# Kernel optimization log

Measured on AMD Instinct MI355X. Metric: run time of the kernel, lower is better.

## Reference

```python
import jax, jax.numpy as jnp
import numpy as np
from jax.scipy.special import logsumexp

EPS_SINK = 0.1
N_ITERS = 100
LN_EPS = 1e-5
ANAT_W = (1.0, 1.0, 1.2)  # anatomical_weights[0:3] used by _get_region_weights
GRIDS = ((5, 0.2), (15, 0.3), (25, 0.5))  # (grid_size, scale_weight)


def layernorm(x, g, b):
    m = x.mean(-1, keepdims=True)
    v = ((x - m) ** 2).mean(-1, keepdims=True)
    return (x - m) / jnp.sqrt(v + LN_EPS) * g + b


def spatial_distribution(bb, g):
    # bb: [B, D, 4] in 0..1000 coords -> [B, D, g*g] binary occupancy grid
    B, D, _ = bb.shape
    bc = bb * (g / 1000.0)
    x, y, w, h = bc[..., 0], bc[..., 1], bc[..., 2], bc[..., 3]
    x1 = jnp.maximum(jnp.trunc(x), 0.0)          # max(0, int(x))
    y1 = jnp.maximum(jnp.trunc(y), 0.0)
    x2 = jnp.minimum(jnp.trunc(x + w), g - 1.0)  # min(g-1, int(x+w))
    y2 = jnp.minimum(jnp.trunc(y + h), g - 1.0)
    gi = jnp.arange(g, dtype=bb.dtype)
    row = (gi[None, None, :, None] >= y1[..., None, None]) & (gi[None, None, :, None] <= y2[..., None, None])
    col = (gi[None, None, None, :] >= x1[..., None, None]) & (gi[None, None, None, :] <= x2[..., None, None])
    nz = jnp.any(bc != 0, axis=-1)[..., None, None]
    grid = (row & col & nz).astype(bb.dtype)  # [B, D, g, g]
    return grid.reshape(B, D, g * g)


def emd_pairs(d1, d2, g):
    # d1, d2: [B, P, n] spatial distributions; returns [B, P] pseudo-EMD exactly as source
    yy, xx = jnp.meshgrid(jnp.arange(g), jnp.arange(g), indexing='ij')
    pos = jnp.stack([xx.ravel(), yy.ravel()], axis=1).astype(jnp.float32)
    diff = pos[:, None, :] - pos[None, :, :]
    C = jnp.sqrt((diff * diff).sum(-1))
    C = C / C.max()
    rw = jnp.ones((g, g), jnp.float32)
    rw = rw.at[: g // 3].mul(ANAT_W[0]).at[g // 3 : (2 * g) // 3].mul(ANAT_W[1]).at[(2 * g) // 3 :].mul(ANAT_W[2])
    C = C * rw.ravel()  # broadcast over columns, same as torch C[n,n] * weights[n]
    K = jnp.exp(-C / EPS_SINK)
    logP = jnp.log(d1[..., :, None] + 1e-8)  # [B,P,n,1]
    logQ = jnp.log(d2[..., None, :] + 1e-8)  # [B,P,1,n]

    def step(carry, _):
        u, v = carry
        u = logP - logsumexp(v + K, axis=-1, keepdims=True)
        v = logQ - logsumexp(u + K.T, axis=-2, keepdims=True)
        return (u, v), None

    (u, v), _ = jax.lax.scan(step, (jnp.zeros_like(logP), jnp.zeros_like(logQ)), None, length=N_ITERS)
    Pm = jnp.exp(u + v + K)
    return (Pm * C).sum((-2, -1))


def setup_inputs() -> dict:
    key = jax.random.key(0)
    ks = jax.random.split(key, 6)
    B, D, F, Hd = 1, 14, 768, 256
    features = jax.random.normal(ks[0], (B, D, F), jnp.float32)
    # x,y in [0,800), w,h in [0,200) so boxes stay inside the 0..1000 frame
    bb = jax.random.uniform(ks[1], (B, D, 4), jnp.float32) * jnp.array([800.0, 800.0, 200.0, 200.0])
    return {
        'features': features,
        'bb_coords': bb,
        'w_embed': jax.random.normal(ks[2], (F, Hd), jnp.float32) * 0.02,
        'b_embed': jnp.zeros((Hd,), jnp.float32),
        'g1': jnp.ones((Hd,), jnp.float32),
        'b1': jnp.zeros((Hd,), jnp.float32),
        'gat_W': jax.random.normal(ks[3], (3, Hd, Hd), jnp.float32) * 0.02,
        'gat_b': jnp.zeros((3, Hd), jnp.float32),
        'gat_g': jnp.ones((3, Hd), jnp.float32),
        'gat_bt': jnp.zeros((3, Hd), jnp.float32),
        'w_out': jax.random.normal(ks[4], (Hd, F), jnp.float32) * 0.02,
        'b_out': jnp.zeros((F,), jnp.float32),
        'g2': jnp.ones((F,), jnp.float32),
        'b2': jnp.zeros((F,), jnp.float32),
    }


def reference(features, bb_coords, w_embed, b_embed, g1, b1, gat_W, gat_b, gat_g, gat_bt, w_out, b_out, g2, b2):
    B, D, _ = features.shape
    H = 1  # num_heads (the only shape-consistent value for the source module)
    x = layernorm(features @ w_embed + b_embed, g1, b1)

    # --- EMD-based adjacency over all 91 unordered disease pairs, vectorized ---
    iu, ju = np.triu_indices(D, k=1)
    adj = jnp.zeros((B, D, D), features.dtype)
    for g, sw in GRIDS:
        dist = spatial_distribution(bb_coords, g)            # [B, D, g*g]
        emd = emd_pairs(dist[:, iu], dist[:, ju], g)         # [B, 91]
        adj = adj.at[:, iu, ju].add(sw * emd).at[:, ju, iu].add(sw * emd)
    adj = jax.nn.softmax(adj, axis=-1)

    # --- 3 GAT layers (q=k=v, per source) ---
    attns = []
    for l in range(3):
        h = x @ gat_W[l] + gat_b[l]                          # [B, D, 256]
        hd = h.shape[-1] // H
        q = h.reshape(B, D, H, hd).transpose(0, 2, 1, 3)     # [B, H, D, hd]
        attn = jnp.einsum('bhnd,bhmd->bhnm', q, q) * hd ** -0.5
        attn = jnp.where(adj[:, None] == 0, -jnp.inf, attn)
        attn = jax.nn.softmax(attn, axis=-1)
        o = jnp.einsum('bhnm,bhmd->bhnd', attn, q)
        o = o.transpose(0, 2, 1, 3).reshape(B, D, H * hd)
        x = layernorm(o, gat_g[l], gat_bt[l])
        attns.append(attn.mean(1))
        x = jax.nn.elu(x)

    out = layernorm(x @ w_out + b_out, g2, b2)
    final_attention = jnp.stack(attns).mean(0)
    return out, final_attention
```

## Files before the change

### kernel.cpp

```cpp
#include <hip/hip_runtime.h>
#include <math.h>


#define NWG 16

__device__ __forceinline__ void astore(float* p, float v) {
  __hip_atomic_store(p, v, __ATOMIC_RELAXED, __HIP_MEMORY_SCOPE_AGENT);
}

__device__ __forceinline__ void bar_arrive(int* flags, int slot, int w) {
  asm volatile("s_waitcnt vmcnt(0)" ::: "memory");
  __syncthreads();
  if (threadIdx.x == 0)
    __hip_atomic_store(&flags[slot * NWG + w], 1, __ATOMIC_RELAXED,
                       __HIP_MEMORY_SCOPE_AGENT);
}

__device__ __forceinline__ void bar_wait(int* flags, int slot) {
  if (threadIdx.x < NWG) {
    while (__hip_atomic_load(&flags[slot * NWG + threadIdx.x],
                             __ATOMIC_RELAXED,
                             __HIP_MEMORY_SCOPE_AGENT) == 0)
      __builtin_amdgcn_s_sleep(1);
  }
  __syncthreads();
  asm volatile("" ::: "memory");
}

__global__ __launch_bounds__(1024) void sdg_fused(
    const float* __restrict__ feat, const float* __restrict__ w_embed,
    const float* __restrict__ b_embed, const float* __restrict__ g1,
    const float* __restrict__ b1, const float* __restrict__ gat_W,
    const float* __restrict__ gat_b, const float* __restrict__ gat_g,
    const float* __restrict__ gat_bt, const float* __restrict__ w_out,
    const float* __restrict__ b_out, const float* __restrict__ g2,
    const float* __restrict__ b2, float* __restrict__ out, int* flags,
    float* __restrict__ e_ws, float* __restrict__ h_ws,
    float* __restrict__ gp_ws, float* __restrict__ st1_ws,
    float* __restrict__ st2_ws) {
  const int w = blockIdx.x, tid = threadIdx.x;
  const int w16 = w * 16, w48 = w * 48;
  const int c = tid & 15;
  const int ksl = (tid >> 4) & 15;
  const int rg = tid >> 8;
  const int t2 = tid & 255;

  __shared__ __align__(16) float SA[14592];
  __shared__ __align__(16) float SB[10752];
  __shared__ __align__(16) float Pb[3600];
  __shared__ float Hb[240];
  __shared__ float Gm[224];
  __shared__ float Asm[224];
  __shared__ float aRow[224];
  __shared__ float hm[16];
  __shared__ float Ov[686];
  __shared__ float Mn[14], Rs[14], ps[14], psq[14];

  float* const Fs = SB;
  float* const Xs = SB;

#pragma unroll
  for (int i = 0; i < 3; ++i) {
    const int idx = i * 1024 + tid;
    const int k = idx >> 2, q = (idx & 3) * 4;
    const float4 v = *(const float4*)(&w_embed[k * 256 + w16 + q]);
    SA[k * 19 + q + 0] = v.x;
    SA[k * 19 + q + 1] = v.y;
    SA[k * 19 + q + 2] = v.z;
    SA[k * 19 + q + 3] = v.w;
  }
  for (int i = tid; i < 2688; i += 1024)
    *(float4*)(&Fs[i * 4]) = ((const float4*)feat)[i];
  if (tid < 224) aRow[tid] = 0.f;
  if (tid < 28) Asm[(tid >> 1) * 16 + 14 + (tid & 1)] = 0.f;
  if (tid < 2) hm[14 + tid] = 0.f;
  __syncthreads();

  {
    float acc[4] = {0.f, 0.f, 0.f, 0.f};
    const int r0 = rg * 4, kb = ksl * 48;
#pragma unroll
    for (int ch = 0; ch < 12; ++ch) {
      const int k = kb + ch * 4;
      const float w0 = SA[(k + 0) * 19 + c];
      const float w1 = SA[(k + 1) * 19 + c];
      const float w2 = SA[(k + 2) * 19 + c];
      const float w3 = SA[(k + 3) * 19 + c];
#pragma unroll
      for (int rr = 0; rr < 4; ++rr) {
        const int r = r0 + rr;
        if (r < 14) {
          const float4 xv = *(const float4*)(&Fs[r * 768 + k]);
          acc[rr] = fmaf(
              xv.x, w0, fmaf(xv.y, w1, fmaf(xv.z, w2, fmaf(xv.w, w3, acc[rr]))));
        }
      }
    }
#pragma unroll
    for (int rr = 0; rr < 4; ++rr) {
      const int r = r0 + rr;
      if (r < 14) Pb[ksl * 225 + r * 16 + c] = acc[rr];
    }
  }
  __syncthreads();
  if (tid < 224) {
    const int r = tid >> 4, cc = tid & 15;
    float v = b_embed[w16 + cc];
#pragma unroll
    for (int q = 0; q < 16; ++q) v += Pb[q * 225 + tid];
    astore(&e_ws[r * 256 + w16 + cc], v);
    float sv = v, sq = v * v;
#pragma unroll
    for (int off = 8; off; off >>= 1) {
      sv += __shfl_xor(sv, off, 16);
      sq += __shfl_xor(sq, off, 16);
    }
    if (cc == 0) {
      astore(&st1_ws[w * 28 + r], sv);
      astore(&st1_ws[w * 28 + 14 + r], sq);
    }
  }
  bar_arrive(flags, 0, w);
  {
    const int k = tid >> 2, q = (tid & 3) * 4;
    const float4 v = *(const float4*)(&gat_W[k * 256 + w16 + q]);
    SA[k * 19 + q + 0] = v.x;
    SA[k * 19 + q + 1] = v.y;
    SA[k * 19 + q + 2] = v.z;
    SA[k * 19 + q + 3] = v.w;
  }
  bar_wait(flags, 0);

  if (tid < 224) {
    const int r = tid >> 4, seg = tid & 15;
    float S = st1_ws[seg * 28 + r];
    float Q = st1_ws[seg * 28 + 14 + r];
#pragma unroll
    for (int off = 8; off; off >>= 1) {
      S += __shfl_xor(S, off, 16);
      Q += __shfl_xor(Q, off, 16);
    }
    if (seg == 0) {
      const float m = S * (1.f / 256.f);
      Mn[r] = m;
      Rs[r] = rsqrtf(Q * (1.f / 256.f) - m * m + 1e-5f);
    }
  }
  if (tid < 896) {
    const float4 v = ((const float4*)e_ws)[tid];
    const int idx = tid * 4, r = idx >> 8, cc = idx & 255;
    *(float4*)(&Xs[r * 260 + cc]) = v;
  }
  __syncthreads();
  for (int i = tid; i < 3584; i += 1024) {
    const int r = i >> 8, cc = i & 255;
    Xs[r * 260 + cc] = (Xs[r * 260 + cc] - Mn[r]) * Rs[r] * g1[cc] + b1[cc];
  }
  __syncthreads();

  for (int l = 0; l < 3; ++l) {
    {
      float acc[4] = {0.f, 0.f, 0.f, 0.f};
      const int r0 = rg * 4, kb = ksl * 16;
#pragma unroll
      for (int ch = 0; ch < 4; ++ch) {
        const int k = kb + ch * 4;
        const float w0 = SA[(k + 0) * 19 + c];
        const float w1 = SA[(k + 1) * 19 + c];
        const float w2 = SA[(k + 2) * 19 + c];
        const float w3 = SA[(k + 3) * 19 + c];
#pragma unroll
        for (int rr = 0; rr < 4; ++rr) {
          const int r = r0 + rr;
          if (r < 14) {
            const float4 xv = *(const float4*)(&Xs[r * 260 + k]);
            acc[rr] = fmaf(
                xv.x, w0,
                fmaf(xv.y, w1, fmaf(xv.z, w2, fmaf(xv.w, w3, acc[rr]))));
          }
        }
      }
#pragma unroll
      for (int rr = 0; rr < 4; ++rr) {
        const int r = r0 + rr;
        if (r < 14) Pb[ksl * 225 + r * 16 + c] = acc[rr];
      }
    }
    __syncthreads();
    if (tid < 224) {
      const int r = tid >> 4, cc = tid & 15;
      float v = gat_b[l * 256 + w16 + cc];
#pragma unroll
      for (int q = 0; q < 16; ++q) v += Pb[q * 225 + tid];
      Hb[r * 17 + cc] = v;
      astore(&h_ws[l * 3584 + r * 256 + w16 + cc], v);
      float sv = v;
#pragma unroll
      for (int off = 8; off; off >>= 1) sv += __shfl_xor(sv, off, 16);
      if (cc == 0) astore(&gp_ws[l * 3584 + w * 224 + 196 + r], sv);
    }
    __syncthreads();
    if (tid < 196) {
      const int i = tid / 14, j = tid - i * 14;
      float s = 0.f;
#pragma unroll
      for (int cc = 0; cc < 16; ++cc)
        s = fmaf(Hb[i * 17 + cc], Hb[j * 17 + cc], s);
      astore(&gp_ws[l * 3584 + w * 224 + tid], s);
    }
    bar_arrive(flags, 1 + l, w);
    if (l < 2) {
      const float* Wn = gat_W + (l + 1) * 65536;
      const int k = tid >> 2, q = (tid & 3) * 4;
      const float4 v = *(const float4*)(&Wn[k * 256 + w16 + q]);
      SA[k * 19 + q + 0] = v.x;
      SA[k * 19 + q + 1] = v.y;
      SA[k * 19 + q + 2] = v.z;
      SA[k * 19 + q + 3] = v.w;
    } else {
#pragma unroll
      for (int g = 0; g < 3; ++g) {
        const int k = tid >> 2, q = (tid & 3) * 4;
        const float4 v = *(const float4*)(&w_out[k * 768 + w48 + g * 16 + q]);
        SA[g * 4864 + k * 19 + q + 0] = v.x;
        SA[g * 4864 + k * 19 + q + 1] = v.y;
        SA[g * 4864 + k * 19 + q + 2] = v.z;
        SA[g * 4864 + k * 19 + q + 3] = v.w;
      }
    }
    bar_wait(flags, 1 + l);

    float hv[16];
    hv[14] = 0.f;
    hv[15] = 0.f;
#pragma unroll
    for (int m = 0; m < 14; ++m) hv[m] = h_ws[l * 3584 + m * 256 + t2];
    if (tid < 196) {
      float s = 0.f;
      const float* gpl = gp_ws + l * 3584 + tid;
#pragma unroll
      for (int ww = 0; ww < 16; ++ww) s += gpl[ww * 224];
      const int i = tid / 14, j = tid - i * 14;
      Gm[i * 16 + j] = s;
      Asm[i * 16 + j] = s * 0.0625f;
    } else if (tid < 210) {
      const int m = tid - 196;
      float s = 0.f;
      const float* gpl = gp_ws + l * 3584 + 196 + m;
#pragma unroll
      for (int ww = 0; ww < 16; ++ww) s += gpl[ww * 224];
      hm[m] = s * (1.f / 256.f);
    }
    __syncthreads();
    if (tid < 224) {
      const int r = tid >> 4, j = tid & 15;
      const float lv = (j < 14) ? Asm[r * 16 + j] : -1e30f;
      float mx = lv;
#pragma unroll
      for (int off = 8; off; off >>= 1) mx = fmaxf(mx, __shfl_xor(mx, off, 16));
      float p = (j < 14) ? expf(lv - mx) : 0.f;
      float sm = p;
#pragma unroll
      for (int off = 8; off; off >>= 1) sm += __shfl_xor(sm, off, 16);
      p /= sm;
      if (j < 14) {
        Asm[r * 16 + j] = p;
        aRow[r * 16 + j] += p * (1.f / 3.f);
      }
    }
    __syncthreads();
    float o[4] = {0.f, 0.f, 0.f, 0.f};
#pragma unroll
    for (int mc = 0; mc < 4; ++mc) {
#pragma unroll
      for (int rr = 0; rr < 4; ++rr) {
        const int r = rg * 4 + rr;
        if (r < 14) {
          const float4 a = *(const float4*)(&Asm[r * 16 + mc * 4]);
          o[rr] = fmaf(a.x, hv[mc * 4 + 0],
                       fmaf(a.y, hv[mc * 4 + 1],
                            fmaf(a.z, hv[mc * 4 + 2],
                                 fmaf(a.w, hv[mc * 4 + 3], o[rr]))));
        }
      }
    }
    if (tid < 224) {
      const int r = tid >> 4, j = tid & 15;
      const float aj = Asm[r * 16 + j];
      float tq = 0.f;
      if (j < 14) {
#pragma unroll
        for (int i = 0; i < 14; ++i)
          tq = fmaf(Asm[r * 16 + i], Gm[i * 16 + j], tq);
      }
      float qv = tq * aj;
      float mv = aj * hm[j];
#pragma unroll
      for (int off = 8; off; off >>= 1) {
        qv += __shfl_xor(qv, off, 16);
        mv += __shfl_xor(mv, off, 16);
      }
      if (j == 0) {
        Mn[r] = mv;
        Rs[r] = rsqrtf(qv * (1.f / 256.f) - mv * mv + 1e-5f);
      }
    }
    __syncthreads();
    {
      const float gc = gat_g[l * 256 + t2], bc = gat_bt[l * 256 + t2];
#pragma unroll
      for (int rr = 0; rr < 4; ++rr) {
        const int r = rg * 4 + rr;
        if (r < 14) {
          const float xn = (o[rr] - Mn[r]) * Rs[r] * gc + bc;
          Xs[r * 260 + t2] = xn > 0.f ? xn : expm1f(xn);
        }
      }
      if (l == 2) {
        if (w < 14 && tid < 14)
          out[10752 + w * 14 + tid] = aRow[w * 16 + tid];
        if (tid < 14) {
          ps[tid] = 0.f;
          psq[tid] = 0.f;
        }
      }
    }
    __syncthreads();
  }

  for (int g = 0; g < 3; ++g) {
    {
      float acc[4] = {0.f, 0.f, 0.f, 0.f};
      const int r0 = rg * 4, kb = ksl * 16;
#pragma unroll
      for (int ch = 0; ch < 4; ++ch) {
        const int k = kb + ch * 4;
        const float w0 = SA[g * 4864 + (k + 0) * 19 + c];
        const float w1 = SA[g * 4864 + (k + 1) * 19 + c];
        const float w2 = SA[g * 4864 + (k + 2) * 19 + c];
        const float w3 = SA[g * 4864 + (k + 3) * 19 + c];
#pragma unroll
        for (int rr = 0; rr < 4; ++rr) {
          const int r = r0 + rr;
          if (r < 14) {
            const float4 xv = *(const float4*)(&Xs[r * 260 + k]);
            acc[rr] = fmaf(
                xv.x, w0,
                fmaf(xv.y, w1, fmaf(xv.z, w2, fmaf(xv.w, w3, acc[rr]))));
          }
        }
      }
#pragma unroll
      for (int rr = 0; rr < 4; ++rr) {
        const int r = r0 + rr;
        if (r < 14) Pb[ksl * 225 + r * 16 + c] = acc[rr];
      }
    }
    __syncthreads();
    if (tid < 224) {
      const int r = tid >> 4, cc = tid & 15;
      float v = b_out[w48 + g * 16 + cc];
#pragma unroll
      for (int q = 0; q < 16; ++q) v += Pb[q * 225 + tid];
      Ov[r * 49 + g * 16 + cc] = v;
      float sv = v, sq = v * v;
#pragma unroll
      for (int off = 8; off; off >>= 1) {
        sv += __shfl_xor(sv, off, 16);
        sq += __shfl_xor(sq, off, 16);
      }
      if (cc == 0) {
        ps[r] += sv;
        psq[r] += sq;
      }
    }
    __syncthreads();
  }
  if (tid < 14) {
    astore(&st2_ws[w * 28 + tid], ps[tid]);
    astore(&st2_ws[w * 28 + 14 + tid], psq[tid]);
  }
  bar_arrive(flags, 4, w);
  bar_wait(flags, 4);
  if (tid < 224) {
    const int r = tid >> 4, seg = tid & 15;
    float S = st2_ws[seg * 28 + r];
    float Q = st2_ws[seg * 28 + 14 + r];
#pragma unroll
    for (int off = 8; off; off >>= 1) {
      S += __shfl_xor(S, off, 16);
      Q += __shfl_xor(Q, off, 16);
    }
    if (seg == 0) {
      const float m = S * (1.f / 768.f);
      Mn[r] = m;
      Rs[r] = rsqrtf(Q * (1.f / 768.f) - m * m + 1e-5f);
    }
  }
  __syncthreads();
  if (tid < 224) {
    const int r = tid >> 4, cc = tid & 15;
    const float m = Mn[r], rs = Rs[r];
#pragma unroll
    for (int g = 0; g < 3; ++g) {
      const int col = w48 + g * 16 + cc;
      out[r * 768 + col] =
          (Ov[r * 49 + g * 16 + cc] - m) * rs * g2[col] + b2[col];
    }
  }
}

extern "C" void kernel_launch(void* const* d_in, const int* in_sizes, int n_in,
                              void* d_out, int out_size, void* d_ws,
                              size_t ws_size, hipStream_t stream) {
  const float* feat = (const float*)d_in[0];
  const float* w_embed = (const float*)d_in[2];
  const float* b_embed = (const float*)d_in[3];
  const float* g1 = (const float*)d_in[4];
  const float* b1 = (const float*)d_in[5];
  const float* gat_W = (const float*)d_in[6];
  const float* gat_b = (const float*)d_in[7];
  const float* gat_g = (const float*)d_in[8];
  const float* gat_bt = (const float*)d_in[9];
  const float* w_out = (const float*)d_in[10];
  const float* b_out = (const float*)d_in[11];
  const float* g2 = (const float*)d_in[12];
  const float* b2 = (const float*)d_in[13];
  float* out = (float*)d_out;

  int* flags = (int*)d_ws;
  float* e_ws = (float*)d_ws + 96;
  float* h_ws = e_ws + 3584;
  float* gp_ws = h_ws + 3 * 3584;
  float* st1_ws = gp_ws + 3 * 3584;
  float* st2_ws = st1_ws + 448;

  hipMemsetAsync(flags, 0, 96 * sizeof(int), stream);
  sdg_fused<<<NWG, 1024, 0, stream>>>(feat, w_embed, b_embed, g1, b1, gat_W,
                                      gat_b, gat_g, gat_bt, w_out, b_out, g2,
                                      b2, out, flags, e_ws, h_ws, gp_ws,
                                      st1_ws, st2_ws);
}
```

Before: 40.89 us.

## Split fused kernel across 32 workgroups with 8-column slices

Doubles the number of cooperating workgroups from 16 to 32, so each handles 8 output columns instead of 16. The K-split doubles to 32 slices and the partial-sum, workspace and flag layouts are resized to match. The aim is to spread the per-block weight loads and matmul work over more compute units, so each block has less serial work. In exchange, every grid barrier has to wait on twice as many blocks, each cross-block reduction reads twice as many partials, and fewer threads per block do useful work.

```diff
diff --git a/kernel.cpp b/kernel.cpp
--- a/kernel.cpp
+++ b/kernel.cpp
@@ -2,7 +2,7 @@
 #include <math.h>
 
 
-#define NWG 16
+#define NWG 32
 
 __device__ __forceinline__ void astore(float* p, float v) {
   __hip_atomic_store(p, v, __ATOMIC_RELAXED, __HIP_MEMORY_SCOPE_AGENT);
@@ -39,35 +39,37 @@
     float* __restrict__ gp_ws, float* __restrict__ st1_ws,
     float* __restrict__ st2_ws) {
   const int w = blockIdx.x, tid = threadIdx.x;
-  const int w16 = w * 16, w48 = w * 48;
-  const int c = tid & 15;
-  const int ksl = (tid >> 4) & 15;
+  const int w8 = w * 8, w24 = w * 24;
+  const int c = tid & 7;
+  const int ksl = (tid >> 3) & 31;
   const int rg = tid >> 8;
   const int t2 = tid & 255;
 
-  __shared__ __align__(16) float SA[14592];
+  __shared__ __align__(16) float SA[6912];
   __shared__ __align__(16) float SB[10752];
-  __shared__ __align__(16) float Pb[3600];
-  __shared__ float Hb[240];
+  __shared__ __align__(16) float Pb[3616];
+  __shared__ float Hb[126];
   __shared__ float Gm[224];
   __shared__ float Asm[224];
   __shared__ float aRow[224];
   __shared__ float hm[16];
-  __shared__ float Ov[686];
+  __shared__ float Ov[350];
   __shared__ float Mn[14], Rs[14], ps[14], psq[14];
 
   float* const Fs = SB;
   float* const Xs = SB;
 
 #pragma unroll
-  for (int i = 0; i < 3; ++i) {
+  for (int i = 0; i < 2; ++i) {
     const int idx = i * 1024 + tid;
-    const int k = idx >> 2, q = (idx & 3) * 4;
-    const float4 v = *(const float4*)(&w_embed[k * 256 + w16 + q]);
-    SA[k * 19 + q + 0] = v.x;
-    SA[k * 19 + q + 1] = v.y;
-    SA[k * 19 + q + 2] = v.z;
-    SA[k * 19 + q + 3] = v.w;
+    if (idx < 1536) {
+      const int k = idx >> 1, q = (idx & 1) * 4;
+      const float4 v = *(const float4*)(&w_embed[k * 256 + w8 + q]);
+      SA[k * 9 + q + 0] = v.x;
+      SA[k * 9 + q + 1] = v.y;
+      SA[k * 9 + q + 2] = v.z;
+      SA[k * 9 + q + 3] = v.w;
+    }
   }
   for (int i = tid; i < 2688; i += 1024)
     *(float4*)(&Fs[i * 4]) = ((const float4*)feat)[i];
@@ -78,14 +80,14 @@
 
   {
     float acc[4] = {0.f, 0.f, 0.f, 0.f};
-    const int r0 = rg * 4, kb = ksl * 48;
-#pragma unroll
-    for (int ch = 0; ch < 12; ++ch) {
+    const int r0 = rg * 4, kb = ksl * 24;
+#pragma unroll
+    for (int ch = 0; ch < 6; ++ch) {
       const int k = kb + ch * 4;
-      const float w0 = SA[(k + 0) * 19 + c];
-      const float w1 = SA[(k + 1) * 19 + c];
-      const float w2 = SA[(k + 2) * 19 + c];
-      const float w3 = SA[(k + 3) * 19 + c];
+      const float w0 = SA[(k + 0) * 9 + c];
+      const float w1 = SA[(k + 1) * 9 + c];
+      const float w2 = SA[(k + 2) * 9 + c];
+      const float w3 = SA[(k + 3) * 9 + c];
 #pragma unroll
       for (int rr = 0; rr < 4; ++rr) {
         const int r = r0 + rr;
@@ -99,21 +101,21 @@
 #pragma unroll
     for (int rr = 0; rr < 4; ++rr) {
       const int r = r0 + rr;
-      if (r < 14) Pb[ksl * 225 + r * 16 + c] = acc[rr];
-    }
-  }
-  __syncthreads();
-  if (tid < 224) {
-    const int r = tid >> 4, cc = tid & 15;
-    float v = b_embed[w16 + cc];
-#pragma unroll
-    for (int q = 0; q < 16; ++q) v += Pb[q * 225 + tid];
-    astore(&e_ws[r * 256 + w16 + cc], v);
+      if (r < 14) Pb[ksl * 113 + r * 8 + c] = acc[rr];
+    }
+  }
+  __syncthreads();
+  if (tid < 112) {
+    const int r = tid >> 3, cc = tid & 7;
+    float v = b_embed[w8 + cc];
+#pragma unroll
+    for (int q = 0; q < 32; ++q) v += Pb[q * 113 + tid];
+    astore(&e_ws[r * 256 + w8 + cc], v);
     float sv = v, sq = v * v;
 #pragma unroll
-    for (int off = 8; off; off >>= 1) {
-      sv += __shfl_xor(sv, off, 16);
-      sq += __shfl_xor(sq, off, 16);
+    for (int off = 4; off; off >>= 1) {
+      sv += __shfl_xor(sv, off, 8);
+      sq += __shfl_xor(sq, off, 8);
     }
     if (cc == 0) {
       astore(&st1_ws[w * 28 + r], sv);
@@ -121,24 +123,24 @@
     }
   }
   bar_arrive(flags, 0, w);
-  {
-    const int k = tid >> 2, q = (tid & 3) * 4;
-    const float4 v = *(const float4*)(&gat_W[k * 256 + w16 + q]);
-    SA[k * 19 + q + 0] = v.x;
-    SA[k * 19 + q + 1] = v.y;
-    SA[k * 19 + q + 2] = v.z;
-    SA[k * 19 + q + 3] = v.w;
+  if (tid < 512) {
+    const int k = tid >> 1, q = (tid & 1) * 4;
+    const float4 v = *(const float4*)(&gat_W[k * 256 + w8 + q]);
+    SA[k * 9 + q + 0] = v.x;
+    SA[k * 9 + q + 1] = v.y;
+    SA[k * 9 + q + 2] = v.z;
+    SA[k * 9 + q + 3] = v.w;
   }
   bar_wait(flags, 0);
 
-  if (tid < 224) {
-    const int r = tid >> 4, seg = tid & 15;
+  if (tid < 448) {
+    const int r = tid >> 5, seg = tid & 31;
     float S = st1_ws[seg * 28 + r];
     float Q = st1_ws[seg * 28 + 14 + r];
 #pragma unroll
-    for (int off = 8; off; off >>= 1) {
-      S += __shfl_xor(S, off, 16);
-      Q += __shfl_xor(Q, off, 16);
+    for (int off = 16; off; off >>= 1) {
+      S += __shfl_xor(S, off, 32);
+      Q += __shfl_xor(Q, off, 32);
     }
     if (seg == 0) {
       const float m = S * (1.f / 256.f);
@@ -161,14 +163,14 @@
   for (int l = 0; l < 3; ++l) {
     {
       float acc[4] = {0.f, 0.f, 0.f, 0.f};
-      const int r0 = rg * 4, kb = ksl * 16;
-#pragma unroll
-      for (int ch = 0; ch < 4; ++ch) {
+      const int r0 = rg * 4, kb = ksl * 8;
+#pragma unroll
+      for (int ch = 0; ch < 2; ++ch) {
         const int k = kb + ch * 4;
-        const float w0 = SA[(k + 0) * 19 + c];
-        const float w1 = SA[(k + 1) * 19 + c];
-        const float w2 = SA[(k + 2) * 19 + c];
-        const float w3 = SA[(k + 3) * 19 + c];
+        const float w0 = SA[(k + 0) * 9 + c];
+        const float w1 = SA[(k + 1) * 9 + c];
+        const float w2 = SA[(k + 2) * 9 + c];
+        const float w3 = SA[(k + 3) * 9 + c];
 #pragma unroll
         for (int rr = 0; rr < 4; ++rr) {
           const int r = r0 + rr;
@@ -183,49 +185,53 @@
 #pragma unroll
       for (int rr = 0; rr < 4; ++rr) {
         const int r = r0 + rr;
-        if (r < 14) Pb[ksl * 225 + r * 16 + c] = acc[rr];
-      }
-    }
-    __syncthreads();
-    if (tid < 224) {
-      const int r = tid >> 4, cc = tid & 15;
-      float v = gat_b[l * 256 + w16 + cc];
-#pragma unroll
-      for (int q = 0; q < 16; ++q) v += Pb[q * 225 + tid];
-      Hb[r * 17 + cc] = v;
-      astore(&h_ws[l * 3584 + r * 256 + w16 + cc], v);
+        if (r < 14) Pb[ksl * 113 + r * 8 + c] = acc[rr];
+      }
+    }
+    __syncthreads();
+    if (tid < 112) {
+      const int r = tid >> 3, cc = tid & 7;
+      float v = gat_b[l * 256 + w8 + cc];
+#pragma unroll
+      for (int q = 0; q < 32; ++q) v += Pb[q * 113 + tid];
+      Hb[r * 9 + cc] = v;
+      astore(&h_ws[l * 3584 + r * 256 + w8 + cc], v);
       float sv = v;
 #pragma unroll
-      for (int off = 8; off; off >>= 1) sv += __shfl_xor(sv, off, 16);
-      if (cc == 0) astore(&gp_ws[l * 3584 + w * 224 + 196 + r], sv);
+      for (int off = 4; off; off >>= 1) sv += __shfl_xor(sv, off, 8);
+      if (cc == 0) astore(&gp_ws[l * 7168 + w * 224 + 196 + r], sv);
     }
     __syncthreads();
     if (tid < 196) {
       const int i = tid / 14, j = tid - i * 14;
       float s = 0.f;
 #pragma unroll
-      for (int cc = 0; cc < 16; ++cc)
-        s = fmaf(Hb[i * 17 + cc], Hb[j * 17 + cc], s);
-      astore(&gp_ws[l * 3584 + w * 224 + tid], s);
+      for (int cc = 0; cc < 8; ++cc)
+        s = fmaf(Hb[i * 9 + cc], Hb[j * 9 + cc], s);
+      astore(&gp_ws[l * 7168 + w * 224 + tid], s);
     }
     bar_arrive(flags, 1 + l, w);
     if (l < 2) {
-      const float* Wn = gat_W + (l + 1) * 65536;
-      const int k = tid >> 2, q = (tid & 3) * 4;
-      const float4 v = *(const float4*)(&Wn[k * 256 + w16 + q]);
-      SA[k * 19 + q + 0] = v.x;
-      SA[k * 19 + q + 1] = v.y;
-      SA[k * 19 + q + 2] = v.z;
-      SA[k * 19 + q + 3] = v.w;
+      if (tid < 512) {
+        const float* Wn = gat_W + (l + 1) * 65536;
+        const int k = tid >> 1, q = (tid & 1) * 4;
+        const float4 v = *(const float4*)(&Wn[k * 256 + w8 + q]);
+        SA[k * 9 + q + 0] = v.x;
+        SA[k * 9 + q + 1] = v.y;
+        SA[k * 9 + q + 2] = v.z;
+        SA[k * 9 + q + 3] = v.w;
+      }
     } else {
-#pragma unroll
-      for (int g = 0; g < 3; ++g) {
-        const int k = tid >> 2, q = (tid & 3) * 4;
-        const float4 v = *(const float4*)(&w_out[k * 768 + w48 + g * 16 + q]);
-        SA[g * 4864 + k * 19 + q + 0] = v.x;
-        SA[g * 4864 + k * 19 + q + 1] = v.y;
-        SA[g * 4864 + k * 19 + q + 2] = v.z;
-        SA[g * 4864 + k * 19 + q + 3] = v.w;
+      if (tid < 512) {
+        const int k = tid >> 1, q = (tid & 1) * 4;
+#pragma unroll
+        for (int g = 0; g < 3; ++g) {
+          const float4 v = *(const float4*)(&w_out[k * 768 + w24 + g * 8 + q]);
+          SA[g * 2304 + k * 9 + q + 0] = v.x;
+          SA[g * 2304 + k * 9 + q + 1] = v.y;
+          SA[g * 2304 + k * 9 + q + 2] = v.z;
+          SA[g * 2304 + k * 9 + q + 3] = v.w;
+        }
       }
     }
     bar_wait(flags, 1 + l);
@@ -237,18 +243,18 @@
     for (int m = 0; m < 14; ++m) hv[m] = h_ws[l * 3584 + m * 256 + t2];
     if (tid < 196) {
       float s = 0.f;
-      const float* gpl = gp_ws + l * 3584 + tid;
-#pragma unroll
-      for (int ww = 0; ww < 16; ++ww) s += gpl[ww * 224];
+      const float* gpl = gp_ws + l * 7168 + tid;
+#pragma unroll
+      for (int ww = 0; ww < 32; ++ww) s += gpl[ww * 224];
       const int i = tid / 14, j = tid - i * 14;
       Gm[i * 16 + j] = s;
       Asm[i * 16 + j] = s * 0.0625f;
     } else if (tid < 210) {
       const int m = tid - 196;
       float s = 0.f;
-      const float* gpl = gp_ws + l * 3584 + 196 + m;
-#pragma unroll
-      for (int ww = 0; ww < 16; ++ww) s += gpl[ww * 224];
+      const float* gpl = gp_ws + l * 7168 + 196 + m;
+#pragma unroll
+      for (int ww = 0; ww < 32; ++ww) s += gpl[ww * 224];
       hm[m] = s * (1.f / 256.f);
     }
     __syncthreads();
@@ -331,14 +337,14 @@
   for (int g = 0; g < 3; ++g) {
     {
       float acc[4] = {0.f, 0.f, 0.f, 0.f};
-      const int r0 = rg * 4, kb = ksl * 16;
-#pragma unroll
-      for (int ch = 0; ch < 4; ++ch) {
+      const int r0 = rg * 4, kb = ksl * 8;
+#pragma unroll
+      for (int ch = 0; ch < 2; ++ch) {
         const int k = kb + ch * 4;
-        const float w0 = SA[g * 4864 + (k + 0) * 19 + c];
-        const float w1 = SA[g * 4864 + (k + 1) * 19 + c];
-        const float w2 = SA[g * 4864 + (k + 2) * 19 + c];
-        const float w3 = SA[g * 4864 + (k + 3) * 19 + c];
+        const float w0 = SA[g * 2304 + (k + 0) * 9 + c];
+        const float w1 = SA[g * 2304 + (k + 1) * 9 + c];
+        const float w2 = SA[g * 2304 + (k + 2) * 9 + c];
+        const float w3 = SA[g * 2304 + (k + 3) * 9 + c];
 #pragma unroll
         for (int rr = 0; rr < 4; ++rr) {
           const int r = r0 + rr;
@@ -353,21 +359,21 @@
 #pragma unroll
       for (int rr = 0; rr < 4; ++rr) {
         const int r = r0 + rr;
-        if (r < 14) Pb[ksl * 225 + r * 16 + c] = acc[rr];
-      }
-    }
-    __syncthreads();
-    if (tid < 224) {
-      const int r = tid >> 4, cc = tid & 15;
-      float v = b_out[w48 + g * 16 + cc];
-#pragma unroll
-      for (int q = 0; q < 16; ++q) v += Pb[q * 225 + tid];
-      Ov[r * 49 + g * 16 + cc] = v;
+        if (r < 14) Pb[ksl * 113 + r * 8 + c] = acc[rr];
+      }
+    }
+    __syncthreads();
+    if (tid < 112) {
+      const int r = tid >> 3, cc = tid & 7;
+      float v = b_out[w24 + g * 8 + cc];
+#pragma unroll
+      for (int q = 0; q < 32; ++q) v += Pb[q * 113 + tid];
+      Ov[r * 25 + g * 8 + cc] = v;
       float sv = v, sq = v * v;
 #pragma unroll
-      for (int off = 8; off; off >>= 1) {
-        sv += __shfl_xor(sv, off, 16);
-        sq += __shfl_xor(sq, off, 16);
+      for (int off = 4; off; off >>= 1) {
+        sv += __shfl_xor(sv, off, 8);
+        sq += __shfl_xor(sq, off, 8);
       }
       if (cc == 0) {
         ps[r] += sv;
@@ -382,14 +388,14 @@
   }
   bar_arrive(flags, 4, w);
   bar_wait(flags, 4);
-  if (tid < 224) {
-    const int r = tid >> 4, seg = tid & 15;
+  if (tid < 448) {
+    const int r = tid >> 5, seg = tid & 31;
     float S = st2_ws[seg * 28 + r];
     float Q = st2_ws[seg * 28 + 14 + r];
 #pragma unroll
-    for (int off = 8; off; off >>= 1) {
-      S += __shfl_xor(S, off, 16);
-      Q += __shfl_xor(Q, off, 16);
+    for (int off = 16; off; off >>= 1) {
+      S += __shfl_xor(S, off, 32);
+      Q += __shfl_xor(Q, off, 32);
     }
     if (seg == 0) {
       const float m = S * (1.f / 768.f);
@@ -398,14 +404,14 @@
     }
   }
   __syncthreads();
-  if (tid < 224) {
-    const int r = tid >> 4, cc = tid & 15;
+  if (tid < 112) {
+    const int r = tid >> 3, cc = tid & 7;
     const float m = Mn[r], rs = Rs[r];
 #pragma unroll
     for (int g = 0; g < 3; ++g) {
-      const int col = w48 + g * 16 + cc;
+      const int col = w24 + g * 8 + cc;
       out[r * 768 + col] =
-          (Ov[r * 49 + g * 16 + cc] - m) * rs * g2[col] + b2[col];
+          (Ov[r * 25 + g * 8 + cc] - m) * rs * g2[col] + b2[col];
     }
   }
 }
@@ -429,13 +435,13 @@
   float* out = (float*)d_out;
 
   int* flags = (int*)d_ws;
-  float* e_ws = (float*)d_ws + 96;
+  float* e_ws = (float*)d_ws + 192;
   float* h_ws = e_ws + 3584;
   float* gp_ws = h_ws + 3 * 3584;
-  float* st1_ws = gp_ws + 3 * 3584;
-  float* st2_ws = st1_ws + 448;
-
-  hipMemsetAsync(flags, 0, 96 * sizeof(int), stream);
+  float* st1_ws = gp_ws + 3 * 7168;
+  float* st2_ws = st1_ws + 896;
+
+  hipMemsetAsync(flags, 0, 192 * sizeof(int), stream);
   sdg_fused<<<NWG, 1024, 0, stream>>>(feat, w_embed, b_embed, g1, b1, gat_W,
                                       gat_b, gat_g, gat_bt, w_out, b_out, g2,
                                       b2, out, flags, e_ws, h_ws, gp_ws,
```

New measurement: 39.02 us. 4.6% less time.
